# Kernel tuning notes

Hardware: AMD Instinct MI355X
Metric: run time of the kernel (lower is better)

Reference implementation:

```python
import jax, jax.numpy as jnp
import numpy as np

N = 8192        # num nodes
F_IN = 256      # input feature dim
HEADS = 4
HEAD_DIM = 64   # out_dim // heads = 256 // 4
NEG_SLOPE = 0.2 # standard GAT LeakyReLU slope


def setup_inputs() -> dict:
    key = jax.random.key(0)
    k1, k2, k3, k4, k5 = jax.random.split(key, 5)
    x = jax.random.normal(k1, (N, F_IN), dtype=jnp.float32)
    adj = jax.random.randint(k2, (N, N), 0, 2, dtype=jnp.int32)
    # glorot-uniform-ish scale for kernel
    lim = float(np.sqrt(6.0 / (F_IN + HEADS * HEAD_DIM)))
    W = jax.random.uniform(k3, (F_IN, HEADS, HEAD_DIM), dtype=jnp.float32, minval=-lim, maxval=lim)
    a_src = jax.random.normal(k4, (HEADS, HEAD_DIM), dtype=jnp.float32) * 0.1
    a_dst = jax.random.normal(k5, (HEADS, HEAD_DIM), dtype=jnp.float32) * 0.1
    bias = jnp.zeros((HEADS * HEAD_DIM,), dtype=jnp.float32)
    return {"x": x, "adj": adj, "W": W, "a_src": a_src, "a_dst": a_dst, "bias": bias}


def reference(x, adj, W, a_src, a_dst, bias):
    # per-head linear transform: [N, H, D]
    h = jnp.einsum('nf,fhd->nhd', x, W)
    # decomposed attention logits: e_ij = leaky_relu(a_src.h_i + a_dst.h_j)
    src = jnp.einsum('nhd,hd->nh', h, a_src)  # [N, H]
    dst = jnp.einsum('nhd,hd->nh', h, a_dst)  # [N, H]
    e = jax.nn.leaky_relu(src[:, None, :] + dst[None, :, :], NEG_SLOPE)  # [N, N, H]
    mask = adj[:, :, None] > 0
    e = jnp.where(mask, e, jnp.float32(-1e9))
    alpha = jax.nn.softmax(e, axis=1)  # softmax over neighbors j for each target i
    out = jnp.einsum('ijh,jhd->ihd', alpha, h)  # aggregate neighbor features
    return out.reshape(N, HEADS * HEAD_DIM) + bias  # concat heads + bias
```

## Files before the change

kernel.cpp:

```cpp
#include <hip/hip_runtime.h>
#include <cstdint>
#include <cstddef>

#define NN 8192
#define HEADS 4

typedef __attribute__((ext_vector_type(4))) float  f4;
typedef __attribute__((ext_vector_type(4))) int    i4;
typedef __attribute__((ext_vector_type(8))) short  short8;
typedef __attribute__((ext_vector_type(4))) unsigned short us4;
typedef __attribute__((ext_vector_type(4))) unsigned int   u4;
typedef __attribute__((ext_vector_type(2))) unsigned int   u2;
typedef unsigned int uint32;

__device__ __forceinline__ unsigned short f2bf(float f) {
    unsigned int u = __builtin_bit_cast(unsigned int, f);
    u += 0x7FFFu + ((u >> 16) & 1u);
    return (unsigned short)(u >> 16);
}

__global__ void k0_convert(const float* __restrict__ x, const float* __restrict__ W,
                           unsigned short* __restrict__ xb, unsigned short* __restrict__ WT) {
    int b = blockIdx.x;
    if (b < 2048) {
        int idx = (b * 256 + threadIdx.x) * 4;
        f4 v = *(const f4*)(x + idx);
        us4 o;
        o.x = f2bf(v.x); o.y = f2bf(v.y); o.z = f2bf(v.z); o.w = f2bf(v.w);
        *(us4*)(xb + idx) = o;
    } else {
        int f = b - 2048;
        int c = threadIdx.x;
        WT[c * 256 + f] = f2bf(W[f * 256 + c]);
    }
}

__global__ __launch_bounds__(256) void kpack(const int* __restrict__ adj,
                                             unsigned char* __restrict__ adjF) {
    __shared__ uint32 tile[32 * 66];
    const int itile = blockIdx.x >> 5;
    const int jgrp  = blockIdx.x & 31;
    const int i0 = itile * 32;
    const int j0 = jgrp * 256;
    const int tid = threadIdx.x;
    const int rrow = tid >> 6;
    const int jc   = (tid & 63) * 4;

    #pragma unroll
    for (int it = 0; it < 8; ++it) {
        int row = it * 4 + rrow;
        i4 v = __builtin_nontemporal_load(
            (const i4*)(adj + (size_t)(i0 + row) * NN + j0 + jc));
        uint32 w = (v.x ? 0xFFu : 0u) | (v.y ? 0xFF00u : 0u) |
                   (v.z ? 0xFF0000u : 0u) | (v.w ? 0xFF000000u : 0u);
        tile[row * 66 + (jc >> 2)] = w;
    }
    __syncthreads();

    const size_t bbase = (size_t)(itile * 256 + jgrp * 8) * 1024;
    #pragma unroll
    for (int k = 0; k < 4; ++k) {
        int s    = k * 256 + tid;
        int jbl  = s >> 7;
        int r    = (s >> 6) & 1;
        int lane = s & 63;
        int col  = lane & 15, quad = lane >> 4;
        int row  = r * 16 + col;
        int c    = jbl * 8 + quad * 2;
        uint32 w0 = tile[row * 66 + c];
        uint32 w1 = tile[row * 66 + c + 1];
        __builtin_nontemporal_store(u2{w0, w1}, (u2*)(adjF + bbase + (size_t)s * 8));
    }
}

__global__ __launch_bounds__(256) void k1_hgemm(
    const unsigned short* __restrict__ xb, const unsigned short* __restrict__ WT,
    const float* __restrict__ aS, const float* __restrict__ aD,
    unsigned short* __restrict__ hF,
    float* __restrict__ sE, float* __restrict__ sE2,
    float* __restrict__ dE, float* __restrict__ dE2)
{
    const int tid  = threadIdx.x;
    const int head = tid >> 6;
    const int lane = tid & 63;
    const int col  = lane & 15;
    const int quad = lane >> 4;
    const int i0   = blockIdx.x * 32;

    const unsigned short* ar0 = xb + (size_t)(i0 + col) * 256 + quad * 8;
    const unsigned short* ar1 = ar0 + 16 * 256;
    const unsigned short* br  = WT + (size_t)(head * 64 + col) * 256 + quad * 8;

    f4 C[2][4];
    #pragma unroll
    for (int a = 0; a < 2; a++)
        #pragma unroll
        for (int b = 0; b < 4; b++) C[a][b] = f4{0.f, 0.f, 0.f, 0.f};

    #pragma unroll
    for (int kk = 0; kk < 256; kk += 32) {
        short8 a0 = *(const short8*)(ar0 + kk);
        short8 a1 = *(const short8*)(ar1 + kk);
        #pragma unroll
        for (int nt = 0; nt < 4; nt++) {
            short8 bf = *(const short8*)(br + nt * 16 * 256 + kk);
            C[0][nt] = __builtin_amdgcn_mfma_f32_16x16x32_bf16(a0, bf, C[0][nt], 0, 0, 0);
            C[1][nt] = __builtin_amdgcn_mfma_f32_16x16x32_bf16(a1, bf, C[1][nt], 0, 0, 0);
        }
    }

    float as_[4], ad_[4];
    #pragma unroll
    for (int nt = 0; nt < 4; nt++) {
        as_[nt] = aS[head * 64 + nt * 16 + col];
        ad_[nt] = aD[head * 64 + nt * 16 + col];
    }
    #pragma unroll
    for (int mt = 0; mt < 2; mt++) {
        #pragma unroll
        for (int r = 0; r < 4; r++) {
            float sv = 0.f, dv = 0.f;
            #pragma unroll
            for (int nt = 0; nt < 4; nt++) {
                sv += C[mt][nt][r] * as_[nt];
                dv += C[mt][nt][r] * ad_[nt];
            }
            #pragma unroll
            for (int m = 1; m < 16; m <<= 1) {
                sv += __shfl_xor(sv, m, 64);
                dv += __shfl_xor(dv, m, 64);
            }
            if (col == 0) {
                int i = i0 + mt * 16 + quad * 4 + r;
                float zs = sv * 1.4426950408889634f;
                float zd = dv * 1.4426950408889634f;
                sE [head * NN + i] = __builtin_amdgcn_exp2f(zs);
                sE2[head * NN + i] = __builtin_amdgcn_exp2f(0.2f * zs);
                dE [head * NN + i] = __builtin_amdgcn_exp2f(zd);
                dE2[head * NN + i] = __builtin_amdgcn_exp2f(0.2f * zd);
            }
        }
    }

    const size_t fbase = (((size_t)blockIdx.x * HEADS + head) * 4) * 512;
    #pragma unroll
    for (int mt = 0; mt < 2; mt++) {
        #pragma unroll
        for (int nt = 0; nt < 4; nt++) {
            #pragma unroll
            for (int r = 0; r < 4; r++) {
                int il = mt * 16 + quad * 4 + r;
                int qp = il >> 3;
                int t  = il & 7;
                hF[fbase + (size_t)nt * 512 + (qp * 16 + col) * 8 + t] =
                    f2bf(C[mt][nt][r]);
            }
        }
    }
}

__device__ __forceinline__ short8 build_w(const u2& ab,
                                          const f4& alo, const f4& ahi,
                                          const f4& blo, const f4& bhi,
                                          float es, float es2) {
    f4 esv  = f4{es, es, es, es};
    f4 es2v = f4{es2, es2, es2, es2};
    f4 x0 = esv * alo,  x1 = esv * ahi;
    f4 y0 = es2v * blo, y1 = es2v * bhi;
    f4 m0 = __builtin_elementwise_max(x0, y0);
    f4 m1 = __builtin_elementwise_max(x1, y1);
    float mm[8] = {m0[0], m0[1], m0[2], m0[3], m1[0], m1[1], m1[2], m1[3]};
    u4 pv;
    #pragma unroll
    for (int k = 0; k < 4; ++k) {
        uint32 src = (k < 2) ? ab.x : ab.y;
        uint32 sel = (k & 1) ? 0x07070606u : 0x05050404u;
        uint32 mkw = __builtin_amdgcn_perm(src, 0u, sel);
        uint32 e0 = __builtin_bit_cast(uint32, mm[2 * k])     + 0x8000u;
        uint32 e1 = __builtin_bit_cast(uint32, mm[2 * k + 1]) + 0x8000u;
        uint32 packed = __builtin_amdgcn_perm(e1, e0, 0x07060302u);
        pv[k] = packed & mkw;
    }
    return __builtin_bit_cast(short8, pv);
}

__global__ __launch_bounds__(256, 4) void k2_gat(
    const unsigned char* __restrict__ adjF, const unsigned short* __restrict__ hF,
    const float* __restrict__ sE, const float* __restrict__ sE2,
    const float* __restrict__ dE, const float* __restrict__ dE2,
    float* __restrict__ Pout, float* __restrict__ PS, int jchunk, int splitBits)
{
    const int tid   = threadIdx.x;
    const int head  = tid >> 6;
    const int lane  = tid & 63;
    const int col   = lane & 15;
    const int quad  = lane >> 4;
    const int split = blockIdx.x & ((1 << splitBits) - 1);
    const int itile = blockIdx.x >> splitBits;
    const int i0    = itile * 32;
    const int j0    = split * jchunk;

    const float es0  = sE [head * NN + i0 + col];
    const float es0b = sE2[head * NN + i0 + col];
    const float es1  = sE [head * NN + i0 + 16 + col];
    const float es1b = sE2[head * NN + i0 + 16 + col];

    const unsigned char* abase =
        adjF + (size_t)(itile * 256 + (j0 >> 5)) * 1024 + lane * 8;
    const float* dEp  = dE  + head * NN + j0 + quad * 8;
    const float* dE2p = dE2 + head * NN + j0 + quad * 8;
    const unsigned short* hbase =
        hF + ((size_t)(j0 >> 5) * HEADS + head) * 4 * 512 + lane * 8;

    f4 acc[2][4];
    f4 accS[2];
    #pragma unroll
    for (int a = 0; a < 2; a++) {
        accS[a] = f4{0.f, 0.f, 0.f, 0.f};
        #pragma unroll
        for (int b = 0; b < 4; b++) acc[a][b] = f4{0.f, 0.f, 0.f, 0.f};
    }
    short8 ones;
    #pragma unroll
    for (int t = 0; t < 8; t++) ones[t] = (short)0x3F80;

    const int ngrp = jchunk >> 5;
    #pragma unroll 4
    for (int g = 0; g < ngrp; ++g) {
        u2 a0 = __builtin_nontemporal_load((const u2*)(abase + (size_t)g * 1024));
        u2 a1 = __builtin_nontemporal_load((const u2*)(abase + (size_t)g * 1024 + 512));
        f4 alo = *(const f4*)(dEp  + g * 32);
        f4 ahi = *(const f4*)(dEp  + g * 32 + 4);
        f4 blo = *(const f4*)(dE2p + g * 32);
        f4 bhi = *(const f4*)(dE2p + g * 32 + 4);
        const unsigned short* hp = hbase + (size_t)g * (HEADS * 4 * 512);
        short8 B0 = *(const short8*)(hp);
        short8 B1 = *(const short8*)(hp + 512);
        short8 B2 = *(const short8*)(hp + 1024);
        short8 B3 = *(const short8*)(hp + 1536);

        short8 af0 = build_w(a0, alo, ahi, blo, bhi, es0, es0b);
        short8 af1 = build_w(a1, alo, ahi, blo, bhi, es1, es1b);

        acc[0][0] = __builtin_amdgcn_mfma_f32_16x16x32_bf16(af0, B0, acc[0][0], 0, 0, 0);
        acc[0][1] = __builtin_amdgcn_mfma_f32_16x16x32_bf16(af0, B1, acc[0][1], 0, 0, 0);
        acc[0][2] = __builtin_amdgcn_mfma_f32_16x16x32_bf16(af0, B2, acc[0][2], 0, 0, 0);
        acc[0][3] = __builtin_amdgcn_mfma_f32_16x16x32_bf16(af0, B3, acc[0][3], 0, 0, 0);
        accS[0]   = __builtin_amdgcn_mfma_f32_16x16x32_bf16(af0, ones, accS[0], 0, 0, 0);
        acc[1][0] = __builtin_amdgcn_mfma_f32_16x16x32_bf16(af1, B0, acc[1][0], 0, 0, 0);
        acc[1][1] = __builtin_amdgcn_mfma_f32_16x16x32_bf16(af1, B1, acc[1][1], 0, 0, 0);
        acc[1][2] = __builtin_amdgcn_mfma_f32_16x16x32_bf16(af1, B2, acc[1][2], 0, 0, 0);
        acc[1][3] = __builtin_amdgcn_mfma_f32_16x16x32_bf16(af1, B3, acc[1][3], 0, 0, 0);
        accS[1]   = __builtin_amdgcn_mfma_f32_16x16x32_bf16(af1, ones, accS[1], 0, 0, 0);
    }

    #pragma unroll
    for (int mt = 0; mt < 2; mt++) {
        #pragma unroll
        for (int nt = 0; nt < 4; nt++) {
            #pragma unroll
            for (int r = 0; r < 4; r++) {
                int row = i0 + mt * 16 + quad * 4 + r;
                __builtin_nontemporal_store(acc[mt][nt][r],
                    Pout + ((size_t)split * NN + row) * 256 + head * 64 + nt * 16 + col);
            }
        }
        if (col == 0) {
            #pragma unroll
            for (int r = 0; r < 4; r++) {
                int row = i0 + mt * 16 + quad * 4 + r;
                __builtin_nontemporal_store(accS[mt][r],
                    PS + ((size_t)split * NN + row) * HEADS + head);
            }
        }
    }
}

__global__ void k3_norm(const float* __restrict__ Pout, const float* __restrict__ PS,
                        const float* __restrict__ bias, float* __restrict__ out,
                        int jsplit)
{
    int t  = blockIdx.x * 256 + threadIdx.x;
    int c4 = t * 4;
    int i    = c4 >> 8;
    int cb   = c4 & 255;
    int head = cb >> 6;
    f4 num = f4{0.f, 0.f, 0.f, 0.f};
    float den = 0.f;
    for (int s = 0; s < jsplit; s++) {
        num += __builtin_nontemporal_load(
            (const f4*)(Pout + ((size_t)s * NN + i) * 256 + cb));
        den += PS[((size_t)s * NN + i) * HEADS + head];
    }
    f4 bv = *(const f4*)(bias + cb);
    f4 o  = num * (1.0f / den) + bv;
    __builtin_nontemporal_store(o, (f4*)(out + c4));
}

extern "C" void kernel_launch(void* const* d_in, const int* in_sizes, int n_in,
                              void* d_out, int out_size, void* d_ws, size_t ws_size,
                              hipStream_t stream) {
    (void)in_sizes; (void)n_in; (void)out_size;
    const float* x    = (const float*)d_in[0];
    const int*   adj  = (const int*)d_in[1];
    const float* W    = (const float*)d_in[2];
    const float* aS   = (const float*)d_in[3];
    const float* aD   = (const float*)d_in[4];
    const float* bias = (const float*)d_in[5];
    float* out = (float*)d_out;

    char* ws = (char*)d_ws;
    unsigned short* xb = (unsigned short*)(ws);
    unsigned short* WT = (unsigned short*)(ws +  4194304);
    unsigned short* hF = (unsigned short*)(ws +  4325376);
    float*  sE   = (float*)(ws +  8519680);
    float*  sE2  = (float*)(ws +  8650752);
    float*  dE   = (float*)(ws +  8781824);
    float*  dE2  = (float*)(ws +  8912896);
    unsigned char* adjF = (unsigned char*)(ws + 9043968);
    float*  PS   = (float*)(ws + 76152832);
    float*  Pout = (float*)(ws + 77201408);

    const size_t need8 = 77201408ull + 8ull * 8388608ull;
    const int splitBits = (ws_size >= need8) ? 3 : 2;
    const int jsplit = 1 << splitBits;
    const int jchunk = NN / jsplit;

    k0_convert<<<2304, 256, 0, stream>>>(x, W, xb, WT);
    kpack<<<8192, 256, 0, stream>>>(adj, adjF);
    k1_hgemm<<<256, 256, 0, stream>>>(xb, WT, aS, aD, hF, sE, sE2, dE, dE2);
    k2_gat<<<256 * jsplit, 256, 0, stream>>>(adjF, hF, sE, sE2, dE, dE2, Pout, PS,
                                             jchunk, splitBits);
    k3_norm<<<2048, 256, 0, stream>>>(Pout, PS, bias, out, jsplit);
}
```

Before: 523.4 us.

## Widen GAT aggregation tile to 64 rows per block, repacking adjacency to match

```diff
diff --git a/kernel.cpp b/kernel.cpp
--- a/kernel.cpp
+++ b/kernel.cpp
@@ -4,6 +4,8 @@
 
 #define NN 8192
 #define HEADS 4
+#define JSPLIT 8
+#define JCHUNK (NN / JSPLIT)
 
 typedef __attribute__((ext_vector_type(4))) float  f4;
 typedef __attribute__((ext_vector_type(4))) int    i4;
@@ -37,39 +39,42 @@
 
 __global__ __launch_bounds__(256) void kpack(const int* __restrict__ adj,
                                              unsigned char* __restrict__ adjF) {
-    __shared__ uint32 tile[32 * 66];
-    const int itile = blockIdx.x >> 5;
-    const int jgrp  = blockIdx.x & 31;
-    const int i0 = itile * 32;
-    const int j0 = jgrp * 256;
+    __shared__ uint32 tile[64][33];
+    const int it64 = blockIdx.x >> 6;
+    const int jgrp = blockIdx.x & 63;
+    const int i0 = it64 * 64;
+    const int j0 = jgrp * 128;
     const int tid = threadIdx.x;
-    const int rrow = tid >> 6;
-    const int jc   = (tid & 63) * 4;
-
-    #pragma unroll
-    for (int it = 0; it < 8; ++it) {
-        int row = it * 4 + rrow;
+    const int rrow = tid >> 5;
+    const int jd   = tid & 31;
+
+    #pragma unroll
+    for (int p = 0; p < 8; ++p) {
+        int row = p * 8 + rrow;
         i4 v = __builtin_nontemporal_load(
-            (const i4*)(adj + (size_t)(i0 + row) * NN + j0 + jc));
+            (const i4*)(adj + (size_t)(i0 + row) * NN + j0 + jd * 4));
         uint32 w = (v.x ? 0xFFu : 0u) | (v.y ? 0xFF00u : 0u) |
                    (v.z ? 0xFF0000u : 0u) | (v.w ? 0xFF000000u : 0u);
-        tile[row * 66 + (jc >> 2)] = w;
+        tile[row][jd] = w;
     }
     __syncthreads();
 
-    const size_t bbase = (size_t)(itile * 256 + jgrp * 8) * 1024;
-    #pragma unroll
-    for (int k = 0; k < 4; ++k) {
-        int s    = k * 256 + tid;
-        int jbl  = s >> 7;
-        int r    = (s >> 6) & 1;
-        int lane = s & 63;
+    const size_t obase = ((size_t)it64 * 256 + jgrp * 4) * 2048;
+    #pragma unroll
+    for (int p = 0; p < 2; ++p) {
+        int idx  = p * 256 + tid;
+        int g    = idx >> 7;
+        int rem  = idx & 127;
+        int lane = rem >> 1;
+        int h    = rem & 1;
         int col  = lane & 15, quad = lane >> 4;
-        int row  = r * 16 + col;
-        int c    = jbl * 8 + quad * 2;
-        uint32 w0 = tile[row * 66 + c];
-        uint32 w1 = tile[row * 66 + c + 1];
-        __builtin_nontemporal_store(u2{w0, w1}, (u2*)(adjF + bbase + (size_t)s * 8));
+        int jb0  = g * 8 + quad * 2;
+        uint32 d0 = tile[(h * 2 + 0) * 16 + col][jb0 + 0];
+        uint32 d1 = tile[(h * 2 + 0) * 16 + col][jb0 + 1];
+        uint32 d2 = tile[(h * 2 + 1) * 16 + col][jb0 + 0];
+        uint32 d3 = tile[(h * 2 + 1) * 16 + col][jb0 + 1];
+        __builtin_nontemporal_store(u4{d0, d1, d2, d3},
+            (u4*)(adjF + obase + (size_t)(g * 64 + lane) * 32 + h * 16));
     }
 }
 
@@ -184,38 +189,40 @@
     return __builtin_bit_cast(short8, pv);
 }
 
-__global__ __launch_bounds__(256, 4) void k2_gat(
+__global__ __launch_bounds__(256, 3) void k2_gat(
     const unsigned char* __restrict__ adjF, const unsigned short* __restrict__ hF,
     const float* __restrict__ sE, const float* __restrict__ sE2,
     const float* __restrict__ dE, const float* __restrict__ dE2,
-    float* __restrict__ Pout, float* __restrict__ PS, int jchunk, int splitBits)
+    float* __restrict__ Pout, float* __restrict__ PS)
 {
     const int tid   = threadIdx.x;
     const int head  = tid >> 6;
     const int lane  = tid & 63;
     const int col   = lane & 15;
     const int quad  = lane >> 4;
-    const int split = blockIdx.x & ((1 << splitBits) - 1);
-    const int itile = blockIdx.x >> splitBits;
-    const int i0    = itile * 32;
-    const int j0    = split * jchunk;
-
-    const float es0  = sE [head * NN + i0 + col];
-    const float es0b = sE2[head * NN + i0 + col];
-    const float es1  = sE [head * NN + i0 + 16 + col];
-    const float es1b = sE2[head * NN + i0 + 16 + col];
+    const int split = blockIdx.x & (JSPLIT - 1);
+    const int it64  = blockIdx.x >> 3;
+    const int i0    = it64 * 64;
+    const int j0    = split * JCHUNK;
+
+    float es_[4], es2_[4];
+    #pragma unroll
+    for (int rf = 0; rf < 4; ++rf) {
+        es_ [rf] = sE [head * NN + i0 + rf * 16 + col];
+        es2_[rf] = sE2[head * NN + i0 + rf * 16 + col];
+    }
 
     const unsigned char* abase =
-        adjF + (size_t)(itile * 256 + (j0 >> 5)) * 1024 + lane * 8;
+        adjF + ((size_t)(it64 * 256 + split * 32) * 64 + lane) * 32;
     const float* dEp  = dE  + head * NN + j0 + quad * 8;
     const float* dE2p = dE2 + head * NN + j0 + quad * 8;
     const unsigned short* hbase =
-        hF + ((size_t)(j0 >> 5) * HEADS + head) * 4 * 512 + lane * 8;
-
-    f4 acc[2][4];
-    f4 accS[2];
-    #pragma unroll
-    for (int a = 0; a < 2; a++) {
+        hF + ((size_t)(split * 32) * HEADS + head) * 4 * 512 + lane * 8;
+
+    f4 acc[4][4];
+    f4 accS[4];
+    #pragma unroll
+    for (int a = 0; a < 4; a++) {
         accS[a] = f4{0.f, 0.f, 0.f, 0.f};
         #pragma unroll
         for (int b = 0; b < 4; b++) acc[a][b] = f4{0.f, 0.f, 0.f, 0.f};
@@ -224,11 +231,10 @@
     #pragma unroll
     for (int t = 0; t < 8; t++) ones[t] = (short)0x3F80;
 
-    const int ngrp = jchunk >> 5;
-    #pragma unroll 4
-    for (int g = 0; g < ngrp; ++g) {
-        u2 a0 = __builtin_nontemporal_load((const u2*)(abase + (size_t)g * 1024));
-        u2 a1 = __builtin_nontemporal_load((const u2*)(abase + (size_t)g * 1024 + 512));
+    for (int g = 0; g < 32; ++g) {
+        const unsigned char* ap = abase + (size_t)g * 2048;
+        u4 awA = __builtin_nontemporal_load((const u4*)(ap));
+        u4 awB = __builtin_nontemporal_load((const u4*)(ap + 16));
         f4 alo = *(const f4*)(dEp  + g * 32);
         f4 ahi = *(const f4*)(dEp  + g * 32 + 4);
         f4 blo = *(const f4*)(dE2p + g * 32);
@@ -239,37 +245,49 @@
         short8 B2 = *(const short8*)(hp + 1024);
         short8 B3 = *(const short8*)(hp + 1536);
 
-        short8 af0 = build_w(a0, alo, ahi, blo, bhi, es0, es0b);
-        short8 af1 = build_w(a1, alo, ahi, blo, bhi, es1, es1b);
+        short8 af0 = build_w(u2{awA.x, awA.y}, alo, ahi, blo, bhi, es_[0], es2_[0]);
+        short8 af1 = build_w(u2{awA.z, awA.w}, alo, ahi, blo, bhi, es_[1], es2_[1]);
+        short8 af2 = build_w(u2{awB.x, awB.y}, alo, ahi, blo, bhi, es_[2], es2_[2]);
+        short8 af3 = build_w(u2{awB.z, awB.w}, alo, ahi, blo, bhi, es_[3], es2_[3]);
 
         acc[0][0] = __builtin_amdgcn_mfma_f32_16x16x32_bf16(af0, B0, acc[0][0], 0, 0, 0);
+        acc[1][0] = __builtin_amdgcn_mfma_f32_16x16x32_bf16(af1, B0, acc[1][0], 0, 0, 0);
+        acc[2][0] = __builtin_amdgcn_mfma_f32_16x16x32_bf16(af2, B0, acc[2][0], 0, 0, 0);
+        acc[3][0] = __builtin_amdgcn_mfma_f32_16x16x32_bf16(af3, B0, acc[3][0], 0, 0, 0);
         acc[0][1] = __builtin_amdgcn_mfma_f32_16x16x32_bf16(af0, B1, acc[0][1], 0, 0, 0);
+        acc[1][1] = __builtin_amdgcn_mfma_f32_16x16x32_bf16(af1, B1, acc[1][1], 0, 0, 0);
+        acc[2][1] = __builtin_amdgcn_mfma_f32_16x16x32_bf16(af2, B1, acc[2][1], 0, 0, 0);
+        acc[3][1] = __builtin_amdgcn_mfma_f32_16x16x32_bf16(af3, B1, acc[3][1], 0, 0, 0);
         acc[0][2] = __builtin_amdgcn_mfma_f32_16x16x32_bf16(af0, B2, acc[0][2], 0, 0, 0);
+        acc[1][2] = __builtin_amdgcn_mfma_f32_16x16x32_bf16(af1, B2, acc[1][2], 0, 0, 0);
+        acc[2][2] = __builtin_amdgcn_mfma_f32_16x16x32_bf16(af2, B2, acc[2][2], 0, 0, 0);
+        acc[3][2] = __builtin_amdgcn_mfma_f32_16x16x32_bf16(af3, B2, acc[3][2], 0, 0, 0);
         acc[0][3] = __builtin_amdgcn_mfma_f32_16x16x32_bf16(af0, B3, acc[0][3], 0, 0, 0);
+        acc[1][3] = __builtin_amdgcn_mfma_f32_16x16x32_bf16(af1, B3, acc[1][3], 0, 0, 0);
+        acc[2][3] = __builtin_amdgcn_mfma_f32_16x16x32_bf16(af2, B3, acc[2][3], 0, 0, 0);
+        acc[3][3] = __builtin_amdgcn_mfma_f32_16x16x32_bf16(af3, B3, acc[3][3], 0, 0, 0);
         accS[0]   = __builtin_amdgcn_mfma_f32_16x16x32_bf16(af0, ones, accS[0], 0, 0, 0);
-        acc[1][0] = __builtin_amdgcn_mfma_f32_16x16x32_bf16(af1, B0, acc[1][0], 0, 0, 0);
-        acc[1][1] = __builtin_amdgcn_mfma_f32_16x16x32_bf16(af1, B1, acc[1][1], 0, 0, 0);
-        acc[1][2] = __builtin_amdgcn_mfma_f32_16x16x32_bf16(af1, B2, acc[1][2], 0, 0, 0);
-        acc[1][3] = __builtin_amdgcn_mfma_f32_16x16x32_bf16(af1, B3, acc[1][3], 0, 0, 0);
         accS[1]   = __builtin_amdgcn_mfma_f32_16x16x32_bf16(af1, ones, accS[1], 0, 0, 0);
-    }
-
-    #pragma unroll
-    for (int mt = 0; mt < 2; mt++) {
+        accS[2]   = __builtin_amdgcn_mfma_f32_16x16x32_bf16(af2, ones, accS[2], 0, 0, 0);
+        accS[3]   = __builtin_amdgcn_mfma_f32_16x16x32_bf16(af3, ones, accS[3], 0, 0, 0);
+    }
+
+    #pragma unroll
+    for (int rf = 0; rf < 4; rf++) {
         #pragma unroll
         for (int nt = 0; nt < 4; nt++) {
             #pragma unroll
             for (int r = 0; r < 4; r++) {
-                int row = i0 + mt * 16 + quad * 4 + r;
-                __builtin_nontemporal_store(acc[mt][nt][r],
+                int row = i0 + rf * 16 + quad * 4 + r;
+                __builtin_nontemporal_store(acc[rf][nt][r],
                     Pout + ((size_t)split * NN + row) * 256 + head * 64 + nt * 16 + col);
             }
         }
         if (col == 0) {
             #pragma unroll
             for (int r = 0; r < 4; r++) {
-                int row = i0 + mt * 16 + quad * 4 + r;
-                __builtin_nontemporal_store(accS[mt][r],
+                int row = i0 + rf * 16 + quad * 4 + r;
+                __builtin_nontemporal_store(accS[rf][r],
                     PS + ((size_t)split * NN + row) * HEADS + head);
             }
         }
@@ -277,8 +295,7 @@
 }
 
 __global__ void k3_norm(const float* __restrict__ Pout, const float* __restrict__ PS,
-                        const float* __restrict__ bias, float* __restrict__ out,
-                        int jsplit)
+                        const float* __restrict__ bias, float* __restrict__ out)
 {
     int t  = blockIdx.x * 256 + threadIdx.x;
     int c4 = t * 4;
@@ -287,7 +304,8 @@
     int head = cb >> 6;
     f4 num = f4{0.f, 0.f, 0.f, 0.f};
     float den = 0.f;
-    for (int s = 0; s < jsplit; s++) {
+    #pragma unroll
+    for (int s = 0; s < JSPLIT; s++) {
         num += __builtin_nontemporal_load(
             (const f4*)(Pout + ((size_t)s * NN + i) * 256 + cb));
         den += PS[((size_t)s * NN + i) * HEADS + head];
@@ -300,7 +318,7 @@
 extern "C" void kernel_launch(void* const* d_in, const int* in_sizes, int n_in,
                               void* d_out, int out_size, void* d_ws, size_t ws_size,
                               hipStream_t stream) {
-    (void)in_sizes; (void)n_in; (void)out_size;
+    (void)in_sizes; (void)n_in; (void)out_size; (void)ws_size;
     const float* x    = (const float*)d_in[0];
     const int*   adj  = (const int*)d_in[1];
     const float* W    = (const float*)d_in[2];
@@ -321,15 +339,9 @@
     float*  PS   = (float*)(ws + 76152832);
     float*  Pout = (float*)(ws + 77201408);
 
-    const size_t need8 = 77201408ull + 8ull * 8388608ull;
-    const int splitBits = (ws_size >= need8) ? 3 : 2;
-    const int jsplit = 1 << splitBits;
-    const int jchunk = NN / jsplit;
-
     k0_convert<<<2304, 256, 0, stream>>>(x, W, xb, WT);
     kpack<<<8192, 256, 0, stream>>>(adj, adjF);
     k1_hgemm<<<256, 256, 0, stream>>>(xb, WT, aS, aD, hF, sE, sE2, dE, dE2);
-    k2_gat<<<256 * jsplit, 256, 0, stream>>>(adjF, hF, sE, sE2, dE, dE2, Pout, PS,
-                                             jchunk, splitBits);
-    k3_norm<<<2048, 256, 0, stream>>>(Pout, PS, bias, out, jsplit);
-}
+    k2_gat<<<128 * JSPLIT, 256, 0, stream>>>(adjF, hF, sE, sE2, dE, dE2, Pout, PS);
+    k3_norm<<<2048, 256, 0, stream>>>(Pout, PS, bias, out);
+}
```

After: 846.2 us. 1.62x slower.

## Double-buffer GAT aggregation loads and reorder block-to-tile mapping

Applied to the files above, without the earlier changes.

```diff
diff --git a/kernel.cpp b/kernel.cpp
--- a/kernel.cpp
+++ b/kernel.cpp
@@ -184,19 +184,19 @@
     return __builtin_bit_cast(short8, pv);
 }
 
-__global__ __launch_bounds__(256, 4) void k2_gat(
+__global__ __launch_bounds__(256, 3) void k2_gat(
     const unsigned char* __restrict__ adjF, const unsigned short* __restrict__ hF,
     const float* __restrict__ sE, const float* __restrict__ sE2,
     const float* __restrict__ dE, const float* __restrict__ dE2,
-    float* __restrict__ Pout, float* __restrict__ PS, int jchunk, int splitBits)
+    float* __restrict__ Pout, float* __restrict__ PS, int jchunk)
 {
     const int tid   = threadIdx.x;
     const int head  = tid >> 6;
     const int lane  = tid & 63;
     const int col   = lane & 15;
     const int quad  = lane >> 4;
-    const int split = blockIdx.x & ((1 << splitBits) - 1);
-    const int itile = blockIdx.x >> splitBits;
+    const int itile = blockIdx.x & 255;
+    const int split = blockIdx.x >> 8;
     const int i0    = itile * 32;
     const int j0    = split * jchunk;
 
@@ -224,35 +224,52 @@
     #pragma unroll
     for (int t = 0; t < 8; t++) ones[t] = (short)0x3F80;
 
+    u2 a0A, a1A; f4 aloA, ahiA, bloA, bhiA; short8 B0A, B1A, B2A, B3A;
+    u2 a0B, a1B; f4 aloB, ahiB, bloB, bhiB; short8 B0B, B1B, B2B, B3B;
+
+#define FETCH(S, G) do {                                                      \
+        const int g_ = (G);                                                   \
+        a0##S = __builtin_nontemporal_load(                                   \
+            (const u2*)(abase + (size_t)g_ * 1024));                          \
+        a1##S = __builtin_nontemporal_load(                                   \
+            (const u2*)(abase + (size_t)g_ * 1024 + 512));                    \
+        alo##S = *(const f4*)(dEp  + g_ * 32);                                \
+        ahi##S = *(const f4*)(dEp  + g_ * 32 + 4);                            \
+        blo##S = *(const f4*)(dE2p + g_ * 32);                                \
+        bhi##S = *(const f4*)(dE2p + g_ * 32 + 4);                            \
+        const unsigned short* hp_ = hbase + (size_t)g_ * (HEADS * 4 * 512);   \
+        B0##S = *(const short8*)(hp_);                                        \
+        B1##S = *(const short8*)(hp_ + 512);                                  \
+        B2##S = *(const short8*)(hp_ + 1024);                                 \
+        B3##S = *(const short8*)(hp_ + 1536);                                 \
+    } while (0)
+
+#define CONSUME(S) do {                                                       \
+        short8 af0 = build_w(a0##S, alo##S, ahi##S, blo##S, bhi##S, es0, es0b);\
+        short8 af1 = build_w(a1##S, alo##S, ahi##S, blo##S, bhi##S, es1, es1b);\
+        acc[0][0] = __builtin_amdgcn_mfma_f32_16x16x32_bf16(af0, B0##S, acc[0][0], 0, 0, 0);\
+        acc[1][0] = __builtin_amdgcn_mfma_f32_16x16x32_bf16(af1, B0##S, acc[1][0], 0, 0, 0);\
+        acc[0][1] = __builtin_amdgcn_mfma_f32_16x16x32_bf16(af0, B1##S, acc[0][1], 0, 0, 0);\
+        acc[1][1] = __builtin_amdgcn_mfma_f32_16x16x32_bf16(af1, B1##S, acc[1][1], 0, 0, 0);\
+        acc[0][2] = __builtin_amdgcn_mfma_f32_16x16x32_bf16(af0, B2##S, acc[0][2], 0, 0, 0);\
+        acc[1][2] = __builtin_amdgcn_mfma_f32_16x16x32_bf16(af1, B2##S, acc[1][2], 0, 0, 0);\
+        acc[0][3] = __builtin_amdgcn_mfma_f32_16x16x32_bf16(af0, B3##S, acc[0][3], 0, 0, 0);\
+        acc[1][3] = __builtin_amdgcn_mfma_f32_16x16x32_bf16(af1, B3##S, acc[1][3], 0, 0, 0);\
+        accS[0]   = __builtin_amdgcn_mfma_f32_16x16x32_bf16(af0, ones, accS[0], 0, 0, 0);\
+        accS[1]   = __builtin_amdgcn_mfma_f32_16x16x32_bf16(af1, ones, accS[1], 0, 0, 0);\
+    } while (0)
+
     const int ngrp = jchunk >> 5;
-    #pragma unroll 4
-    for (int g = 0; g < ngrp; ++g) {
-        u2 a0 = __builtin_nontemporal_load((const u2*)(abase + (size_t)g * 1024));
-        u2 a1 = __builtin_nontemporal_load((const u2*)(abase + (size_t)g * 1024 + 512));
-        f4 alo = *(const f4*)(dEp  + g * 32);
-        f4 ahi = *(const f4*)(dEp  + g * 32 + 4);
-        f4 blo = *(const f4*)(dE2p + g * 32);
-        f4 bhi = *(const f4*)(dE2p + g * 32 + 4);
-        const unsigned short* hp = hbase + (size_t)g * (HEADS * 4 * 512);
-        short8 B0 = *(const short8*)(hp);
-        short8 B1 = *(const short8*)(hp + 512);
-        short8 B2 = *(const short8*)(hp + 1024);
-        short8 B3 = *(const short8*)(hp + 1536);
-
-        short8 af0 = build_w(a0, alo, ahi, blo, bhi, es0, es0b);
-        short8 af1 = build_w(a1, alo, ahi, blo, bhi, es1, es1b);
-
-        acc[0][0] = __builtin_amdgcn_mfma_f32_16x16x32_bf16(af0, B0, acc[0][0], 0, 0, 0);
-        acc[0][1] = __builtin_amdgcn_mfma_f32_16x16x32_bf16(af0, B1, acc[0][1], 0, 0, 0);
-        acc[0][2] = __builtin_amdgcn_mfma_f32_16x16x32_bf16(af0, B2, acc[0][2], 0, 0, 0);
-        acc[0][3] = __builtin_amdgcn_mfma_f32_16x16x32_bf16(af0, B3, acc[0][3], 0, 0, 0);
-        accS[0]   = __builtin_amdgcn_mfma_f32_16x16x32_bf16(af0, ones, accS[0], 0, 0, 0);
-        acc[1][0] = __builtin_amdgcn_mfma_f32_16x16x32_bf16(af1, B0, acc[1][0], 0, 0, 0);
-        acc[1][1] = __builtin_amdgcn_mfma_f32_16x16x32_bf16(af1, B1, acc[1][1], 0, 0, 0);
-        acc[1][2] = __builtin_amdgcn_mfma_f32_16x16x32_bf16(af1, B2, acc[1][2], 0, 0, 0);
-        acc[1][3] = __builtin_amdgcn_mfma_f32_16x16x32_bf16(af1, B3, acc[1][3], 0, 0, 0);
-        accS[1]   = __builtin_amdgcn_mfma_f32_16x16x32_bf16(af1, ones, accS[1], 0, 0, 0);
-    }
+    FETCH(A, 0);
+    FETCH(B, 1);
+    for (int g = 0; g < ngrp; g += 2) {
+        CONSUME(A);
+        if (g + 2 < ngrp) FETCH(A, g + 2);
+        CONSUME(B);
+        if (g + 3 < ngrp) FETCH(B, g + 3);
+    }
+#undef FETCH
+#undef CONSUME
 
     #pragma unroll
     for (int mt = 0; mt < 2; mt++) {
@@ -322,14 +339,12 @@
     float*  Pout = (float*)(ws + 77201408);
 
     const size_t need8 = 77201408ull + 8ull * 8388608ull;
-    const int splitBits = (ws_size >= need8) ? 3 : 2;
-    const int jsplit = 1 << splitBits;
+    const int jsplit = (ws_size >= need8) ? 8 : 4;
     const int jchunk = NN / jsplit;
 
     k0_convert<<<2304, 256, 0, stream>>>(x, W, xb, WT);
     kpack<<<8192, 256, 0, stream>>>(adj, adjF);
     k1_hgemm<<<256, 256, 0, stream>>>(xb, WT, aS, aD, hF, sE, sE2, dE, dE2);
-    k2_gat<<<256 * jsplit, 256, 0, stream>>>(adjF, hF, sE, sE2, dE, dE2, Pout, PS,
-                                             jchunk, splitBits);
+    k2_gat<<<256 * jsplit, 256, 0, stream>>>(adjF, hF, sE, sE2, dE, dE2, Pout, PS, jchunk);
     k3_norm<<<2048, 256, 0, stream>>>(Pout, PS, bias, out, jsplit);
 }
```

Result: slower. 548.4 us (+4.8%).
